# Kernel tuning notes

Measured on AMD Instinct MI355X. Metric: run time of the kernel, lower is better.

Reference implementation:

```python
import jax, jax.numpy as jnp
import numpy as np

# ---- static configuration (mirrors init_kwargs) ----
C_IN = 1
SEQ_LEN = 512
N_KERNELS = 10000
KSS = [7, 9, 11]
KS_MAX = max(KSS)
BATCH = 8


def _make_params(seed=42):
    """Replicates the random kernel generation in RocketFeaturesPytorch.__init__."""
    rng = np.random.RandomState(seed)
    ks = np.empty(N_KERNELS, np.int32)
    dil = np.empty(N_KERNELS, np.int32)
    pad = np.empty(N_KERNELS, np.int32)  # per-side padding actually applied (= 2*padding)
    W = np.zeros((N_KERNELS, C_IN, KS_MAX), np.float32)  # zero-padded to KS_MAX taps
    b = np.empty(N_KERNELS, np.float32)
    for i in range(N_KERNELS):
        k = int(rng.choice(KSS))
        d_f = 2.0 ** rng.uniform(0, np.log2((SEQ_LEN - 1) // (k - 1)))
        d = int(d_f)  # Conv1d dilation uses int(dilation)
        p = int((k - 1) * d_f // 2) if rng.randint(2) == 1 else 0  # padding uses FLOAT dilation (as in source)
        w = rng.randn(1, C_IN, k).astype(np.float32)
        w -= w.mean()
        W[i, :, :k] = w[0]
        b[i] = np.float32(2.0 * (rng.rand() - 0.5))
        ks[i], dil[i], pad[i] = k, d, 2 * p  # layer padding = 2*padding per side
    lo = SEQ_LEN + 2 * pad - dil * (ks - 1)  # per-kernel output length (>=1 guaranteed)
    return W, b, ks, dil, pad, lo

_W, _B, _KS, _DIL, _PAD, _LO = _make_params()
PAD_MAX = int(_PAD.max())
T_MAX = int(_LO.max())


def setup_inputs() -> dict:
    key = jax.random.key(0)
    x = jax.random.normal(key, (BATCH, C_IN, SEQ_LEN), dtype=jnp.float32)
    return {
        "x": x,
        "weights": jnp.asarray(_W),                     # [K, C, KS_MAX]
        "biases": jnp.asarray(_B),                      # [K]
        "base": jnp.asarray(PAD_MAX - _PAD, jnp.int32), # [K] start offset into padded x
        "dil": jnp.asarray(_DIL, jnp.int32),            # [K]
        "lo": jnp.asarray(_LO, jnp.int32),              # [K] valid output length
    }


def reference(x, weights, biases, base, dil, lo):
    B, C, L = x.shape
    K = weights.shape[0]
    xpad = jnp.pad(x, ((0, 0), (0, 0), (PAD_MAX, PAD_MAX)))  # [B, C, Lp]
    Lp = xpad.shape[-1]
    t = jnp.arange(T_MAX, dtype=jnp.int32)                   # [T]

    # dilated conv for all kernels at once: out[b,k,t] = sum_{c,j} w[k,c,j] * xpad[b,c, base[k]+t+j*dil[k]]
    acc = jnp.zeros((B, K, T_MAX), x.dtype)
    for j in range(KS_MAX):  # small static loop over taps
        idx = jnp.clip(base[:, None] + t[None, :] + j * dil[:, None], 0, Lp - 1)  # [K, T]
        g = xpad[:, :, idx]                                   # [B, C, K, T]
        acc = acc + jnp.einsum('bckt,kc->bkt', g, weights[:, :, j])
    out = acc + biases[None, :, None]                         # [B, K, T]

    valid = t[None, :] < lo[:, None]                          # [K, T]
    maxs = jnp.max(jnp.where(valid[None], out, -jnp.inf), axis=-1)                       # [B, K]
    ppv = jnp.sum(jnp.where(valid[None], out > 0, False), axis=-1) / lo[None, :].astype(x.dtype)  # [B, K]

    # original interleaves (max_i, ppv_i) per kernel along the feature dim
    return jnp.stack([maxs, ppv.astype(x.dtype)], axis=-1).reshape(B, 2 * K)
```

## Files before the change

kernel.cpp:

```cpp
#include <hip/hip_runtime.h>
#include <math.h>

#define NK      10000
#define LSEQ    512
#define KSMAX   11
#define ROWS_DW (514 * 4)
#define RED_OFF ROWS_DW
#define SM_DW   (ROWS_DW + 256 * 10)

typedef _Float16 half2v __attribute__((ext_vector_type(2)));

union H2U { half2v h; unsigned int u; };

template <int KS>
__device__ __forceinline__ void run_conv(const float4* __restrict__ rows,
                                         const half2v* __restrict__ wh, half2v bb,
                                         int pad, int dl, int lk, int lane,
                                         half2v& m0, half2v& m1, half2v& m2, half2v& m3,
                                         half2v& c0, half2v& c1, half2v& c2, half2v& c3) {
    const half2v one2  = {(_Float16)1.0f, (_Float16)1.0f};
    const half2v zero2 = {(_Float16)0.0f, (_Float16)0.0f};
    const half2v big2  = {(_Float16)16384.0f, (_Float16)16384.0f};
    for (int t0 = 0; t0 < lk; t0 += 64) {
        const int t = t0 + lane;
        half2v a0 = bb, a1 = bb, a2 = bb, a3 = bb;
        int pos = t - pad;
        #pragma unroll
        for (int j = 0; j < KS; ++j) {
            int pc = min(max(pos, -1), LSEQ);
            float4 r = rows[pc + 1];
            half2v wj = wh[j];
            a0 += wj * ((half2v*)&r)[0];
            a1 += wj * ((half2v*)&r)[1];
            a2 += wj * ((half2v*)&r)[2];
            a3 += wj * ((half2v*)&r)[3];
            pos += dl;
        }
        if (t < lk) {
            m0 = __builtin_elementwise_max(m0, a0);
            m1 = __builtin_elementwise_max(m1, a1);
            m2 = __builtin_elementwise_max(m2, a2);
            m3 = __builtin_elementwise_max(m3, a3);
            c0 += __builtin_elementwise_min(__builtin_elementwise_max(a0 * big2, zero2), one2);
            c1 += __builtin_elementwise_min(__builtin_elementwise_max(a1 * big2, zero2), one2);
            c2 += __builtin_elementwise_min(__builtin_elementwise_max(a2 * big2, zero2), one2);
            c3 += __builtin_elementwise_min(__builtin_elementwise_max(a3 * big2, zero2), one2);
        }
    }
}

__global__ __launch_bounds__(256) void rocket_kernel(
    const float* __restrict__ x, const float* __restrict__ W,
    const float* __restrict__ bias, const int* __restrict__ dil,
    const int* __restrict__ lo, float* __restrict__ out) {
    __shared__ __align__(16) float sm[SM_DW];
    const int tid  = threadIdx.x;
    const int wave = tid >> 6;
    const int lane = tid & 63;
    const int k    = blockIdx.x * 4 + wave;

    #pragma unroll
    for (int i = 0; i < 2; ++i) {
        int p = tid + i * 256;
        half2v h0 = {(_Float16)x[0 * LSEQ + p], (_Float16)x[1 * LSEQ + p]};
        half2v h1 = {(_Float16)x[2 * LSEQ + p], (_Float16)x[3 * LSEQ + p]};
        half2v h2 = {(_Float16)x[4 * LSEQ + p], (_Float16)x[5 * LSEQ + p]};
        half2v h3 = {(_Float16)x[6 * LSEQ + p], (_Float16)x[7 * LSEQ + p]};
        float4 v;
        ((half2v*)&v)[0] = h0;
        ((half2v*)&v)[1] = h1;
        ((half2v*)&v)[2] = h2;
        ((half2v*)&v)[3] = h3;
        *(float4*)(sm + (size_t)(p + 1) * 4) = v;
    }
    if (tid < 4)           sm[tid] = 0.0f;
    else if (tid < 8)      sm[513 * 4 + (tid - 4)] = 0.0f;

    float w[KSMAX];
    half2v wh[KSMAX];
    #pragma unroll
    for (int j = 0; j < KSMAX; ++j) {
        w[j] = W[(size_t)k * KSMAX + j];
        _Float16 wf = (_Float16)w[j];
        wh[j] = (half2v){wf, wf};
    }
    _Float16 bf = (_Float16)bias[k];
    const half2v bb = {bf, bf};
    const int dl = dil[k];
    const int lk = lo[k];

    __syncthreads();

    half2v mneg = {(_Float16)(-INFINITY), (_Float16)(-INFINITY)};
    half2v zz   = {(_Float16)0.0f, (_Float16)0.0f};
    half2v m0 = mneg, m1 = mneg, m2 = mneg, m3 = mneg;
    half2v c0 = zz,   c1 = zz,   c2 = zz,   c3 = zz;

    const bool z7 = (w[7] == 0.0f) && (w[8] == 0.0f) && (w[9] == 0.0f) && (w[10] == 0.0f);
    const bool z9 = (w[9] == 0.0f) && (w[10] == 0.0f);
    const float4* rows = (const float4*)sm;
    if (z7) {
        int pad = (lk - LSEQ + dl * 6) >> 1;
        run_conv<7 >(rows, wh, bb, pad, dl, lk, lane, m0, m1, m2, m3, c0, c1, c2, c3);
    } else if (z9) {
        int pad = (lk - LSEQ + dl * 8) >> 1;
        run_conv<9 >(rows, wh, bb, pad, dl, lk, lane, m0, m1, m2, m3, c0, c1, c2, c3);
    } else {
        int pad = (lk - LSEQ + dl * 10) >> 1;
        run_conv<11>(rows, wh, bb, pad, dl, lk, lane, m0, m1, m2, m3, c0, c1, c2, c3);
    }

    {
        unsigned int* red = (unsigned int*)(sm + RED_OFF);
        const int tb = tid * 10;
        H2U u0, u1, u2, u3;
        uint2 p01, p23;
        u0.h = m0; u1.h = m1; u2.h = m2; u3.h = m3;
        p01.x = u0.u; p01.y = u1.u; p23.x = u2.u; p23.y = u3.u;
        *(uint2*)(red + tb + 0) = p01;
        *(uint2*)(red + tb + 2) = p23;
        u0.h = c0; u1.h = c1; u2.h = c2; u3.h = c3;
        p01.x = u0.u; p01.y = u1.u; p23.x = u2.u; p23.y = u3.u;
        *(uint2*)(red + tb + 4) = p01;
        *(uint2*)(red + tb + 6) = p23;

        const int q  = lane & 7;
        const int dv = lane >> 3;
        const bool ismax = dv < 4;
        const int wbase = (tid & ~63) * 10;
        half2v r = ismax ? (half2v){(_Float16)(-INFINITY), (_Float16)(-INFINITY)}
                         : (half2v){(_Float16)0.0f, (_Float16)0.0f};
        #pragma unroll
        for (int i = 0; i < 8; ++i) {
            H2U t;
            t.u = red[wbase + (q + 8 * i) * 10 + dv];
            r = ismax ? __builtin_elementwise_max(r, t.h) : (r + t.h);
        }
        #pragma unroll
        for (int s = 1; s < 8; s <<= 1) {
            H2U me, ot;
            me.h = r;
            ot.u = (unsigned int)__shfl_xor((int)me.u, s, 64);
            r = ismax ? __builtin_elementwise_max(r, ot.h) : (r + ot.h);
        }
        if (q == 0) {
            if (ismax) {
                int b = 2 * dv;
                out[(size_t)b       * (2 * NK) + 2 * k] = (float)r.x;
                out[(size_t)(b + 1) * (2 * NK) + 2 * k] = (float)r.y;
            } else {
                int b = 2 * (dv - 4);
                float inv = 1.0f / (float)lk;
                out[(size_t)b       * (2 * NK) + 2 * k + 1] = (float)r.x * inv;
                out[(size_t)(b + 1) * (2 * NK) + 2 * k + 1] = (float)r.y * inv;
            }
        }
    }
}

extern "C" void kernel_launch(void* const* d_in, const int* in_sizes, int n_in,
                              void* d_out, int out_size, void* d_ws, size_t ws_size,
                              hipStream_t stream) {
    const float* x    = (const float*)d_in[0];
    const float* W    = (const float*)d_in[1];
    const float* bias = (const float*)d_in[2];
    const int*   dil  = (const int*)d_in[4];
    const int*   lo   = (const int*)d_in[5];
    float* out = (float*)d_out;

    rocket_kernel<<<NK / 4, 256, 0, stream>>>(x, W, bias, dil, lo, out);
}
```

Baseline: 84.79 us.

## Bucket kernels by dilation and size so each wave computes four kernels together

Adds a single-block bucketing kernel that sorts the conv kernels by (dilation, kernel size, padding flag) into groups padded to multiples of four. The main kernel then has each wave process four same-dilation kernels at once, sharing each shared-memory row load across four weight sets and masking each kernel's valid output window. The aim is to cut LDS loads per FMA and amortise per-kernel overhead. In exchange it adds an extra serial launch with a scan in one block, extra rows computed where the kernels' windows differ, and higher register pressure.

```diff
diff --git a/kernel.cpp b/kernel.cpp
--- a/kernel.cpp
+++ b/kernel.cpp
@@ -1,50 +1,120 @@
 #include <hip/hip_runtime.h>
 #include <math.h>
 
-#define NK      10000
-#define LSEQ    512
-#define KSMAX   11
-#define ROWS_DW (514 * 4)
-#define RED_OFF ROWS_DW
-#define SM_DW   (ROWS_DW + 256 * 10)
+#define NK        10000
+#define LSEQ      512
+#define KSMAX     11
+#define NKEY      3072
+#define SCAN_N    4096
+#define TOT_SLOT  19456
+#define GRID_MAIN 1216
+#define ROWS_DW   (514 * 4)
+#define RED_OFF   ROWS_DW
+#define SM_DW     (ROWS_DW + 256 * 10)
 
 typedef _Float16 half2v __attribute__((ext_vector_type(2)));
-
 union H2U { half2v h; unsigned int u; };
 
+__device__ __forceinline__ int ks_index(float w7, float w8, float w9, float w10) {
+    if (w7 == 0.f && w8 == 0.f && w9 == 0.f && w10 == 0.f) return 0;
+    if (w9 == 0.f && w10 == 0.f) return 1;
+    return 2;
+}
+
+__global__ __launch_bounds__(1024) void bucket_kernel(
+    const float* __restrict__ W, const int* __restrict__ dil, const int* __restrict__ lo,
+    int* __restrict__ ord) {
+    __shared__ unsigned cnt[NKEY];
+    __shared__ unsigned cur[NKEY];
+    __shared__ unsigned sa[SCAN_N];
+    __shared__ unsigned sb[SCAN_N];
+    const int tid = threadIdx.x;
+    for (int i = tid; i < NKEY; i += 1024) cnt[i] = 0;
+    __syncthreads();
+    for (int i = tid; i < NK; i += 1024) {
+        const float* wr = W + (size_t)i * KSMAX;
+        int ksi = ks_index(wr[7], wr[8], wr[9], wr[10]);
+        int ks = 7 + 2 * ksi;
+        int d = dil[i];
+        int pd = (lo[i] - LSEQ + d * (ks - 1)) > 0;
+        int key = (((d - 1) * 3 + ksi) << 1) | pd;
+        atomicAdd(&cnt[key], 1u);
+    }
+    __syncthreads();
+    for (int i = tid; i < SCAN_N; i += 1024)
+        sa[i] = (i < NKEY) ? ((cnt[i] + 3u) & ~3u) : 0u;
+    __syncthreads();
+    unsigned* A = sa; unsigned* B = sb;
+    for (int off = 1; off < SCAN_N; off <<= 1) {
+        for (int i = tid; i < SCAN_N; i += 1024)
+            B[i] = A[i] + ((i >= off) ? A[i - off] : 0u);
+        unsigned* t = A; A = B; B = t;
+        __syncthreads();
+    }
+    for (int i = tid; i < NKEY; i += 1024)
+        cur[i] = A[i] - ((cnt[i] + 3u) & ~3u);
+    for (int i = tid; i < TOT_SLOT; i += 1024) ord[i] = -1;
+    __syncthreads();
+    for (int i = tid; i < NK; i += 1024) {
+        const float* wr = W + (size_t)i * KSMAX;
+        int ksi = ks_index(wr[7], wr[8], wr[9], wr[10]);
+        int ks = 7 + 2 * ksi;
+        int d = dil[i];
+        int pd = (lo[i] - LSEQ + d * (ks - 1)) > 0;
+        int key = (((d - 1) * 3 + ksi) << 1) | pd;
+        unsigned slot = atomicAdd(&cur[key], 1u);
+        ord[slot] = i;
+    }
+}
+
 template <int KS>
-__device__ __forceinline__ void run_conv(const float4* __restrict__ rows,
-                                         const half2v* __restrict__ wh, half2v bb,
-                                         int pad, int dl, int lk, int lane,
-                                         half2v& m0, half2v& m1, half2v& m2, half2v& m3,
-                                         half2v& c0, half2v& c1, half2v& c2, half2v& c3) {
+__device__ __forceinline__ void run_quad(const float4* __restrict__ rows,
+                                         const half2v (&wh)[4][KSMAX], const half2v (&bb)[4],
+                                         const int (&pq)[4], const int (&lkq)[4],
+                                         int dl, int r_lo, int r_hi, int lane,
+                                         half2v (&m)[4][4], half2v (&c)[4][4]) {
     const half2v one2  = {(_Float16)1.0f, (_Float16)1.0f};
     const half2v zero2 = {(_Float16)0.0f, (_Float16)0.0f};
     const half2v big2  = {(_Float16)16384.0f, (_Float16)16384.0f};
-    for (int t0 = 0; t0 < lk; t0 += 64) {
-        const int t = t0 + lane;
-        half2v a0 = bb, a1 = bb, a2 = bb, a3 = bb;
-        int pos = t - pad;
+    const half2v ninf2 = {(_Float16)(-INFINITY), (_Float16)(-INFINITY)};
+    for (int r0 = r_lo; r0 < r_hi; r0 += 64) {
+        const int r = r0 + lane;
+        half2v a[4][4];
+        #pragma unroll
+        for (int q = 0; q < 4; ++q) {
+            #pragma unroll
+            for (int i = 0; i < 4; ++i) a[q][i] = bb[q];
+        }
+        int pos = r;
         #pragma unroll
         for (int j = 0; j < KS; ++j) {
             int pc = min(max(pos, -1), LSEQ);
-            float4 r = rows[pc + 1];
-            half2v wj = wh[j];
-            a0 += wj * ((half2v*)&r)[0];
-            a1 += wj * ((half2v*)&r)[1];
-            a2 += wj * ((half2v*)&r)[2];
-            a3 += wj * ((half2v*)&r)[3];
+            float4 rr = rows[pc + 1];
+            half2v v0 = ((half2v*)&rr)[0];
+            half2v v1 = ((half2v*)&rr)[1];
+            half2v v2 = ((half2v*)&rr)[2];
+            half2v v3 = ((half2v*)&rr)[3];
+            #pragma unroll
+            for (int q = 0; q < 4; ++q) {
+                half2v wj = wh[q][j];
+                a[q][0] += wj * v0;
+                a[q][1] += wj * v1;
+                a[q][2] += wj * v2;
+                a[q][3] += wj * v3;
+            }
             pos += dl;
         }
-        if (t < lk) {
-            m0 = __builtin_elementwise_max(m0, a0);
-            m1 = __builtin_elementwise_max(m1, a1);
-            m2 = __builtin_elementwise_max(m2, a2);
-            m3 = __builtin_elementwise_max(m3, a3);
-            c0 += __builtin_elementwise_min(__builtin_elementwise_max(a0 * big2, zero2), one2);
-            c1 += __builtin_elementwise_min(__builtin_elementwise_max(a1 * big2, zero2), one2);
-            c2 += __builtin_elementwise_min(__builtin_elementwise_max(a2 * big2, zero2), one2);
-            c3 += __builtin_elementwise_min(__builtin_elementwise_max(a3 * big2, zero2), one2);
+        #pragma unroll
+        for (int q = 0; q < 4; ++q) {
+            unsigned t = (unsigned)(r + pq[q]);
+            bool valid = t < (unsigned)lkq[q];
+            #pragma unroll
+            for (int i = 0; i < 4; ++i) {
+                half2v av = valid ? a[q][i] : ninf2;
+                m[q][i] = __builtin_elementwise_max(m[q][i], av);
+                c[q][i] += __builtin_elementwise_min(
+                               __builtin_elementwise_max(av * big2, zero2), one2);
+            }
         }
     }
 }
@@ -52,12 +122,11 @@
 __global__ __launch_bounds__(256) void rocket_kernel(
     const float* __restrict__ x, const float* __restrict__ W,
     const float* __restrict__ bias, const int* __restrict__ dil,
-    const int* __restrict__ lo, float* __restrict__ out) {
+    const int* __restrict__ lo, const int* __restrict__ ord,
+    float* __restrict__ out) {
     __shared__ __align__(16) float sm[SM_DW];
-    const int tid  = threadIdx.x;
-    const int wave = tid >> 6;
-    const int lane = tid & 63;
-    const int k    = blockIdx.x * 4 + wave;
+    const int tid = threadIdx.x;
+    if (ord[blockIdx.x * 16] < 0) return;
 
     #pragma unroll
     for (int i = 0; i < 2; ++i) {
@@ -76,83 +145,116 @@
     if (tid < 4)           sm[tid] = 0.0f;
     else if (tid < 8)      sm[513 * 4 + (tid - 4)] = 0.0f;
 
-    float w[KSMAX];
-    half2v wh[KSMAX];
-    #pragma unroll
-    for (int j = 0; j < KSMAX; ++j) {
-        w[j] = W[(size_t)k * KSMAX + j];
-        _Float16 wf = (_Float16)w[j];
-        wh[j] = (half2v){wf, wf};
-    }
-    _Float16 bf = (_Float16)bias[k];
-    const half2v bb = {bf, bf};
-    const int dl = dil[k];
-    const int lk = lo[k];
-
-    __syncthreads();
-
-    half2v mneg = {(_Float16)(-INFINITY), (_Float16)(-INFINITY)};
-    half2v zz   = {(_Float16)0.0f, (_Float16)0.0f};
-    half2v m0 = mneg, m1 = mneg, m2 = mneg, m3 = mneg;
-    half2v c0 = zz,   c1 = zz,   c2 = zz,   c3 = zz;
-
-    const bool z7 = (w[7] == 0.0f) && (w[8] == 0.0f) && (w[9] == 0.0f) && (w[10] == 0.0f);
-    const bool z9 = (w[9] == 0.0f) && (w[10] == 0.0f);
+    const int wave = tid >> 6;
+    const int lane = tid & 63;
+
+    int kq[4];
+    #pragma unroll
+    for (int q = 0; q < 4; ++q)
+        kq[q] = __builtin_amdgcn_readfirstlane(ord[blockIdx.x * 16 + wave * 4 + q]);
+
+    half2v wh[4][KSMAX];
+    half2v bb[4];
+    int pq[4], lkq[4];
+    float w7 = 0.f, w8 = 0.f, w9 = 0.f, w10 = 0.f;
+    int dl = 1;
+    bool got = false;
+    #pragma unroll
+    for (int q = 0; q < 4; ++q) {
+        int k = kq[q];
+        if (k >= 0) {
+            const float* wr = W + (size_t)k * KSMAX;
+            #pragma unroll
+            for (int j = 0; j < KSMAX; ++j) {
+                _Float16 wf = (_Float16)wr[j];
+                wh[q][j] = (half2v){wf, wf};
+            }
+            _Float16 bf = (_Float16)bias[k];
+            bb[q] = (half2v){bf, bf};
+            lkq[q] = lo[k];
+            if (!got) { got = true; w7 = wr[7]; w8 = wr[8]; w9 = wr[9]; w10 = wr[10]; dl = dil[k]; }
+        } else {
+            #pragma unroll
+            for (int j = 0; j < KSMAX; ++j) wh[q][j] = (half2v){(_Float16)0.f, (_Float16)0.f};
+            bb[q] = (half2v){(_Float16)0.f, (_Float16)0.f};
+            lkq[q] = 0;
+        }
+    }
+    const int ksi = ks_index(w7, w8, w9, w10);
+    const int ks = 7 + 2 * ksi;
+    int r_lo = 0, r_hi = 0;
+    #pragma unroll
+    for (int q = 0; q < 4; ++q) {
+        if (kq[q] >= 0) {
+            pq[q] = (lkq[q] - LSEQ + dl * (ks - 1)) >> 1;
+            r_lo = min(r_lo, -pq[q]);
+            r_hi = max(r_hi, lkq[q] - pq[q]);
+        } else {
+            pq[q] = 0;
+        }
+    }
+
+    __syncthreads();
+
+    const half2v ninf2 = {(_Float16)(-INFINITY), (_Float16)(-INFINITY)};
+    const half2v zz    = {(_Float16)0.f, (_Float16)0.f};
+    half2v m[4][4], c[4][4];
+    #pragma unroll
+    for (int q = 0; q < 4; ++q) {
+        #pragma unroll
+        for (int i = 0; i < 4; ++i) { m[q][i] = ninf2; c[q][i] = zz; }
+    }
+
     const float4* rows = (const float4*)sm;
-    if (z7) {
-        int pad = (lk - LSEQ + dl * 6) >> 1;
-        run_conv<7 >(rows, wh, bb, pad, dl, lk, lane, m0, m1, m2, m3, c0, c1, c2, c3);
-    } else if (z9) {
-        int pad = (lk - LSEQ + dl * 8) >> 1;
-        run_conv<9 >(rows, wh, bb, pad, dl, lk, lane, m0, m1, m2, m3, c0, c1, c2, c3);
-    } else {
-        int pad = (lk - LSEQ + dl * 10) >> 1;
-        run_conv<11>(rows, wh, bb, pad, dl, lk, lane, m0, m1, m2, m3, c0, c1, c2, c3);
-    }
-
-    {
-        unsigned int* red = (unsigned int*)(sm + RED_OFF);
-        const int tb = tid * 10;
+    if (ksi == 0)      run_quad<7 >(rows, wh, bb, pq, lkq, dl, r_lo, r_hi, lane, m, c);
+    else if (ksi == 1) run_quad<9 >(rows, wh, bb, pq, lkq, dl, r_lo, r_hi, lane, m, c);
+    else               run_quad<11>(rows, wh, bb, pq, lkq, dl, r_lo, r_hi, lane, m, c);
+
+    unsigned int* red = (unsigned int*)(sm + RED_OFF);
+    const int tb = tid * 10;
+    const int wbase = (tid & ~63) * 10;
+    const int sub = lane & 7;
+    const int dv = lane >> 3;
+    const bool ismax = dv < 4;
+    #pragma unroll
+    for (int q = 0; q < 4; ++q) {
+        if (kq[q] < 0) continue;
         H2U u0, u1, u2, u3;
         uint2 p01, p23;
-        u0.h = m0; u1.h = m1; u2.h = m2; u3.h = m3;
+        u0.h = m[q][0]; u1.h = m[q][1]; u2.h = m[q][2]; u3.h = m[q][3];
         p01.x = u0.u; p01.y = u1.u; p23.x = u2.u; p23.y = u3.u;
         *(uint2*)(red + tb + 0) = p01;
         *(uint2*)(red + tb + 2) = p23;
-        u0.h = c0; u1.h = c1; u2.h = c2; u3.h = c3;
+        u0.h = c[q][0]; u1.h = c[q][1]; u2.h = c[q][2]; u3.h = c[q][3];
         p01.x = u0.u; p01.y = u1.u; p23.x = u2.u; p23.y = u3.u;
         *(uint2*)(red + tb + 4) = p01;
         *(uint2*)(red + tb + 6) = p23;
 
-        const int q  = lane & 7;
-        const int dv = lane >> 3;
-        const bool ismax = dv < 4;
-        const int wbase = (tid & ~63) * 10;
-        half2v r = ismax ? (half2v){(_Float16)(-INFINITY), (_Float16)(-INFINITY)}
-                         : (half2v){(_Float16)0.0f, (_Float16)0.0f};
+        half2v r2 = ismax ? ninf2 : zz;
         #pragma unroll
         for (int i = 0; i < 8; ++i) {
             H2U t;
-            t.u = red[wbase + (q + 8 * i) * 10 + dv];
-            r = ismax ? __builtin_elementwise_max(r, t.h) : (r + t.h);
+            t.u = red[wbase + (sub + 8 * i) * 10 + dv];
+            r2 = ismax ? __builtin_elementwise_max(r2, t.h) : (r2 + t.h);
         }
         #pragma unroll
         for (int s = 1; s < 8; s <<= 1) {
             H2U me, ot;
-            me.h = r;
+            me.h = r2;
             ot.u = (unsigned int)__shfl_xor((int)me.u, s, 64);
-            r = ismax ? __builtin_elementwise_max(r, ot.h) : (r + ot.h);
-        }
-        if (q == 0) {
+            r2 = ismax ? __builtin_elementwise_max(r2, ot.h) : (r2 + ot.h);
+        }
+        if (sub == 0) {
+            int kk = kq[q];
             if (ismax) {
                 int b = 2 * dv;
-                out[(size_t)b       * (2 * NK) + 2 * k] = (float)r.x;
-                out[(size_t)(b + 1) * (2 * NK) + 2 * k] = (float)r.y;
+                out[(size_t)b       * (2 * NK) + 2 * kk] = (float)r2.x;
+                out[(size_t)(b + 1) * (2 * NK) + 2 * kk] = (float)r2.y;
             } else {
                 int b = 2 * (dv - 4);
-                float inv = 1.0f / (float)lk;
-                out[(size_t)b       * (2 * NK) + 2 * k + 1] = (float)r.x * inv;
-                out[(size_t)(b + 1) * (2 * NK) + 2 * k + 1] = (float)r.y * inv;
+                float inv = 1.0f / (float)lkq[q];
+                out[(size_t)b       * (2 * NK) + 2 * kk + 1] = (float)r2.x * inv;
+                out[(size_t)(b + 1) * (2 * NK) + 2 * kk + 1] = (float)r2.y * inv;
             }
         }
     }
@@ -167,6 +269,8 @@
     const int*   dil  = (const int*)d_in[4];
     const int*   lo   = (const int*)d_in[5];
     float* out = (float*)d_out;
-
-    rocket_kernel<<<NK / 4, 256, 0, stream>>>(x, W, bias, dil, lo, out);
-}
+    int* ord = (int*)d_ws;
+
+    bucket_kernel<<<1, 1024, 0, stream>>>(W, dil, lo, ord);
+    rocket_kernel<<<GRID_MAIN, 256, 0, stream>>>(x, W, bias, dil, lo, ord, out);
+}
```

Result: slower. 111.3 us (+31.3%).

## Replace static one-kernel-per-wave grid with persistent atomic work-stealing pools

Applied to the files above, without the earlier changes.

Launches a fixed grid of persistent blocks whose waves claim kernels dynamically through atomic counters spread over 32 pools. This spreads the uneven per-kernel cost (different output lengths and tap counts) across waves and avoids repeating the shared-memory staging of x for every 4 kernels. It adds a memset launch, atomic traffic, and a loop with per-kernel weight loads inside the wave.

```diff
diff --git a/kernel.cpp b/kernel.cpp
--- a/kernel.cpp
+++ b/kernel.cpp
@@ -1,15 +1,17 @@
 #include <hip/hip_runtime.h>
 #include <math.h>
 
-#define NK      10000
-#define LSEQ    512
-#define KSMAX   11
-#define ROWS_DW (514 * 4)
-#define RED_OFF ROWS_DW
-#define SM_DW   (ROWS_DW + 256 * 10)
+#define NK       10000
+#define LSEQ     512
+#define KSMAX    11
+#define POOLS    32
+#define CNT_STRIDE 64
+#define GRID_MAIN 2048
+#define ROWS_DW  (514 * 4)
+#define RED_OFF  ROWS_DW
+#define SM_DW    (ROWS_DW + 256 * 10)
 
 typedef _Float16 half2v __attribute__((ext_vector_type(2)));
-
 union H2U { half2v h; unsigned int u; };
 
 template <int KS>
@@ -52,12 +54,13 @@
 __global__ __launch_bounds__(256) void rocket_kernel(
     const float* __restrict__ x, const float* __restrict__ W,
     const float* __restrict__ bias, const int* __restrict__ dil,
-    const int* __restrict__ lo, float* __restrict__ out) {
+    const int* __restrict__ lo, int* __restrict__ cnt,
+    float* __restrict__ out) {
     __shared__ __align__(16) float sm[SM_DW];
     const int tid  = threadIdx.x;
     const int wave = tid >> 6;
     const int lane = tid & 63;
-    const int k    = blockIdx.x * 4 + wave;
+    (void)wave;
 
     #pragma unroll
     for (int i = 0; i < 2; ++i) {
@@ -76,43 +79,58 @@
     if (tid < 4)           sm[tid] = 0.0f;
     else if (tid < 8)      sm[513 * 4 + (tid - 4)] = 0.0f;
 
-    float w[KSMAX];
-    half2v wh[KSMAX];
-    #pragma unroll
-    for (int j = 0; j < KSMAX; ++j) {
-        w[j] = W[(size_t)k * KSMAX + j];
-        _Float16 wf = (_Float16)w[j];
-        wh[j] = (half2v){wf, wf};
-    }
-    _Float16 bf = (_Float16)bias[k];
-    const half2v bb = {bf, bf};
-    const int dl = dil[k];
-    const int lk = lo[k];
-
     __syncthreads();
 
-    half2v mneg = {(_Float16)(-INFINITY), (_Float16)(-INFINITY)};
-    half2v zz   = {(_Float16)0.0f, (_Float16)0.0f};
-    half2v m0 = mneg, m1 = mneg, m2 = mneg, m3 = mneg;
-    half2v c0 = zz,   c1 = zz,   c2 = zz,   c3 = zz;
+    const int pool = blockIdx.x & (POOLS - 1);
+    const int poolsize = (NK - pool + POOLS - 1) / POOLS;
+    int* pc = cnt + pool * CNT_STRIDE;
 
-    const bool z7 = (w[7] == 0.0f) && (w[8] == 0.0f) && (w[9] == 0.0f) && (w[10] == 0.0f);
-    const bool z9 = (w[9] == 0.0f) && (w[10] == 0.0f);
     const float4* rows = (const float4*)sm;
-    if (z7) {
-        int pad = (lk - LSEQ + dl * 6) >> 1;
-        run_conv<7 >(rows, wh, bb, pad, dl, lk, lane, m0, m1, m2, m3, c0, c1, c2, c3);
-    } else if (z9) {
-        int pad = (lk - LSEQ + dl * 8) >> 1;
-        run_conv<9 >(rows, wh, bb, pad, dl, lk, lane, m0, m1, m2, m3, c0, c1, c2, c3);
-    } else {
-        int pad = (lk - LSEQ + dl * 10) >> 1;
-        run_conv<11>(rows, wh, bb, pad, dl, lk, lane, m0, m1, m2, m3, c0, c1, c2, c3);
-    }
+    unsigned int* red = (unsigned int*)(sm + RED_OFF);
+    const int tb = tid * 10;
+    const int wbase = (tid & ~63) * 10;
+    const int sub = lane & 7;
+    const int dv = lane >> 3;
+    const bool ismax = dv < 4;
+    const half2v ninf2 = {(_Float16)(-INFINITY), (_Float16)(-INFINITY)};
+    const half2v zz    = {(_Float16)0.f, (_Float16)0.f};
 
-    {
-        unsigned int* red = (unsigned int*)(sm + RED_OFF);
-        const int tb = tid * 10;
+    while (true) {
+        int n = 0;
+        if (lane == 0) n = atomicAdd(pc, 1);
+        n = __shfl(n, 0, 64);
+        if (n >= poolsize) break;
+        const int k = __builtin_amdgcn_readfirstlane(pool + POOLS * n);
+
+        const float* wr = W + (size_t)k * KSMAX;
+        half2v wh[KSMAX];
+        #pragma unroll
+        for (int j = 0; j < KSMAX; ++j) {
+            _Float16 wf = (_Float16)wr[j];
+            wh[j] = (half2v){wf, wf};
+        }
+        const float w7 = wr[7], w8 = wr[8], w9 = wr[9], w10 = wr[10];
+        _Float16 bf = (_Float16)bias[k];
+        const half2v bb = {bf, bf};
+        const int dl = dil[k];
+        const int lk = lo[k];
+
+        half2v m0 = ninf2, m1 = ninf2, m2 = ninf2, m3 = ninf2;
+        half2v c0 = zz,    c1 = zz,    c2 = zz,    c3 = zz;
+
+        const bool z7 = (w7 == 0.f) && (w8 == 0.f) && (w9 == 0.f) && (w10 == 0.f);
+        const bool z9 = (w9 == 0.f) && (w10 == 0.f);
+        if (z7) {
+            int pad = (lk - LSEQ + dl * 6) >> 1;
+            run_conv<7 >(rows, wh, bb, pad, dl, lk, lane, m0, m1, m2, m3, c0, c1, c2, c3);
+        } else if (z9) {
+            int pad = (lk - LSEQ + dl * 8) >> 1;
+            run_conv<9 >(rows, wh, bb, pad, dl, lk, lane, m0, m1, m2, m3, c0, c1, c2, c3);
+        } else {
+            int pad = (lk - LSEQ + dl * 10) >> 1;
+            run_conv<11>(rows, wh, bb, pad, dl, lk, lane, m0, m1, m2, m3, c0, c1, c2, c3);
+        }
+
         H2U u0, u1, u2, u3;
         uint2 p01, p23;
         u0.h = m0; u1.h = m1; u2.h = m2; u3.h = m3;
@@ -124,35 +142,30 @@
         *(uint2*)(red + tb + 4) = p01;
         *(uint2*)(red + tb + 6) = p23;
 
-        const int q  = lane & 7;
-        const int dv = lane >> 3;
-        const bool ismax = dv < 4;
-        const int wbase = (tid & ~63) * 10;
-        half2v r = ismax ? (half2v){(_Float16)(-INFINITY), (_Float16)(-INFINITY)}
-                         : (half2v){(_Float16)0.0f, (_Float16)0.0f};
+        half2v r2 = ismax ? ninf2 : zz;
         #pragma unroll
         for (int i = 0; i < 8; ++i) {
             H2U t;
-            t.u = red[wbase + (q + 8 * i) * 10 + dv];
-            r = ismax ? __builtin_elementwise_max(r, t.h) : (r + t.h);
+            t.u = red[wbase + (sub + 8 * i) * 10 + dv];
+            r2 = ismax ? __builtin_elementwise_max(r2, t.h) : (r2 + t.h);
         }
         #pragma unroll
         for (int s = 1; s < 8; s <<= 1) {
             H2U me, ot;
-            me.h = r;
+            me.h = r2;
             ot.u = (unsigned int)__shfl_xor((int)me.u, s, 64);
-            r = ismax ? __builtin_elementwise_max(r, ot.h) : (r + ot.h);
+            r2 = ismax ? __builtin_elementwise_max(r2, ot.h) : (r2 + ot.h);
         }
-        if (q == 0) {
+        if (sub == 0) {
             if (ismax) {
                 int b = 2 * dv;
-                out[(size_t)b       * (2 * NK) + 2 * k] = (float)r.x;
-                out[(size_t)(b + 1) * (2 * NK) + 2 * k] = (float)r.y;
+                out[(size_t)b       * (2 * NK) + 2 * k] = (float)r2.x;
+                out[(size_t)(b + 1) * (2 * NK) + 2 * k] = (float)r2.y;
             } else {
                 int b = 2 * (dv - 4);
                 float inv = 1.0f / (float)lk;
-                out[(size_t)b       * (2 * NK) + 2 * k + 1] = (float)r.x * inv;
-                out[(size_t)(b + 1) * (2 * NK) + 2 * k + 1] = (float)r.y * inv;
+                out[(size_t)b       * (2 * NK) + 2 * k + 1] = (float)r2.x * inv;
+                out[(size_t)(b + 1) * (2 * NK) + 2 * k + 1] = (float)r2.y * inv;
             }
         }
     }
@@ -167,6 +180,8 @@
     const int*   dil  = (const int*)d_in[4];
     const int*   lo   = (const int*)d_in[5];
     float* out = (float*)d_out;
+    int* cnt = (int*)d_ws;
 
-    rocket_kernel<<<NK / 4, 256, 0, stream>>>(x, W, bias, dil, lo, out);
+    hipMemsetAsync(cnt, 0, POOLS * CNT_STRIDE * sizeof(int), stream);
+    rocket_kernel<<<GRID_MAIN, 256, 0, stream>>>(x, W, bias, dil, lo, cnt, out);
 }
```

Result: no change. 86.19 us (+1.6%).
